# Kernel tuning notes

Hardware: AMD Instinct MI355X
Metric: run time of the kernel (lower is better)

## Reference

```python
import jax, jax.numpy as jnp
import numpy as np

N_NODES = 50000
N_EDGES = 400000
IN_DIM = 8
HIDDEN = 768
N_LAYERS = 4
LN_EPS = 1e-5


def setup_inputs() -> dict:
    key = jax.random.key(0)
    ks = jax.random.split(key, 10)
    x = jax.random.normal(ks[0], (N_NODES, IN_DIM), dtype=jnp.float32)
    edge_index = jax.random.randint(ks[1], (2, N_EDGES), 0, N_NODES, dtype=jnp.int32)
    # input projection
    s_in = 1.0 / np.sqrt(IN_DIM)
    Wp = jax.random.uniform(ks[2], (HIDDEN, IN_DIM), jnp.float32, -s_in, s_in)
    bp = jax.random.uniform(ks[3], (HIDDEN,), jnp.float32, -s_in, s_in)
    # stacked per-layer SAGEConv params (all layers have out_c == HIDDEN here)
    s_h = 1.0 / np.sqrt(HIDDEN)
    Wl = jax.random.uniform(ks[4], (N_LAYERS, HIDDEN, HIDDEN), jnp.float32, -s_h, s_h)  # lin_l (aggregated neighbors), has bias
    bl = jax.random.uniform(ks[5], (N_LAYERS, HIDDEN), jnp.float32, -s_h, s_h)
    Wr = jax.random.uniform(ks[6], (N_LAYERS, HIDDEN, HIDDEN), jnp.float32, -s_h, s_h)  # lin_r (root), no bias
    # LayerNorm params
    gamma = jnp.ones((N_LAYERS, HIDDEN), dtype=jnp.float32)
    beta = jnp.zeros((N_LAYERS, HIDDEN), dtype=jnp.float32)
    return {"x": x, "Wp": Wp, "bp": bp, "Wl": Wl, "bl": bl, "Wr": Wr,
            "gamma": gamma, "beta": beta, "edge_index": edge_index}


def _layer_norm(h, g, b):
    mu = jnp.mean(h, axis=-1, keepdims=True)
    var = jnp.mean(jnp.square(h - mu), axis=-1, keepdims=True)
    return (h - mu) * jax.lax.rsqrt(var + LN_EPS) * g + b


def reference(x, Wp, bp, Wl, bl, Wr, gamma, beta, edge_index):
    n = x.shape[0]
    src, dst = edge_index[0], edge_index[1]
    # in-degree per target node, clamped for mean
    deg = jax.ops.segment_sum(jnp.ones_like(dst, dtype=x.dtype), dst, num_segments=n)
    inv_deg = 1.0 / jnp.maximum(deg, 1.0)

    h = x @ Wp.T + bp  # [N, HIDDEN]

    def layer(h, params):
        Wl_i, bl_i, Wr_i, g_i, b_i = params
        # mean aggregation of source features at targets: [N, C]
        agg = jax.ops.segment_sum(h[src], dst, num_segments=n) * inv_deg[:, None]
        out = agg @ Wl_i.T + bl_i + h @ Wr_i.T  # SAGEConv
        out = _layer_norm(jax.nn.silu(out), g_i, b_i)  # norm(silu(conv))
        return out, None

    h, _ = jax.lax.scan(layer, h, (Wl, bl, Wr, gamma, beta))
    return h
```

## Files before the change

kernel.cpp:

```cpp
#include <hip/hip_runtime.h>

#define NN 50000
#define NE 400000
#define HID 768
#define NL 4

typedef short bf16x8_t __attribute__((ext_vector_type(8)));
typedef float f32x4_t __attribute__((ext_vector_type(4)));

__device__ __forceinline__ unsigned short f2bf(float f) {
  union { float f; unsigned int u; } c; c.f = f;
  unsigned int u = c.u;
  u += 0x7FFF + ((u >> 16) & 1);
  return (unsigned short)(u >> 16);
}
__device__ __forceinline__ float bf2f(unsigned short s) {
  union { unsigned int u; float f; } c; c.u = ((unsigned int)s) << 16;
  return c.f;
}

__global__ void k_zero2(int* __restrict__ a, int* __restrict__ b, int n) {
  int i = blockIdx.x * blockDim.x + threadIdx.x;
  if (i < n) { a[i] = 0; b[i] = 0; }
}

__global__ void k_cvt(const float* __restrict__ a, unsigned short* __restrict__ o, int n) {
  int i = blockIdx.x * blockDim.x + threadIdx.x;
  if (i < n) o[i] = f2bf(a[i]);
}

__global__ __launch_bounds__(256) void k_inproj(const float* __restrict__ x,
                                                const float* __restrict__ Wp,
                                                const float* __restrict__ bp,
                                                unsigned short* __restrict__ h) {
  int n = blockIdx.x;
  __shared__ float xs[8];
  if (threadIdx.x < 8) xs[threadIdx.x] = x[n * 8 + threadIdx.x];
  __syncthreads();
  for (int j = threadIdx.x; j < HID; j += 256) {
    const float* w = Wp + j * 8;
    float s = bp[j];
#pragma unroll
    for (int k = 0; k < 8; ++k) s += xs[k] * w[k];
    h[(size_t)n * HID + j] = f2bf(s);
  }
}

__global__ void k_deg(const int* __restrict__ dst, int* __restrict__ deg) {
  int i = blockIdx.x * blockDim.x + threadIdx.x;
  if (i < NE) atomicAdd(&deg[dst[i]], 1);
}

__global__ __launch_bounds__(1024) void k_scan(const int* __restrict__ deg, int* __restrict__ rowptr) {
  __shared__ int sm[1024];
  const int chunk = 49;
  int t = threadIdx.x;
  int start = t * chunk;
  int end = min(start + chunk, NN);
  int local = 0;
  for (int i = start; i < end; ++i) local += deg[i];
  sm[t] = local;
  __syncthreads();
  for (int off = 1; off < 1024; off <<= 1) {
    int v = (t >= off) ? sm[t - off] : 0;
    __syncthreads();
    sm[t] += v;
    __syncthreads();
  }
  int run = sm[t] - local;
  for (int i = start; i < end; ++i) { rowptr[i] = run; run += deg[i]; }
  if (start < NN && end == NN) rowptr[NN] = run;
}

__global__ void k_fill(const int* __restrict__ src, const int* __restrict__ dst,
                       const int* __restrict__ rowptr, int* __restrict__ cursor,
                       int* __restrict__ csr) {
  int i = blockIdx.x * blockDim.x + threadIdx.x;
  if (i < NE) {
    int d = dst[i];
    int pos = atomicAdd(&cursor[d], 1);
    csr[rowptr[d] + pos] = src[i];
  }
}

__global__ __launch_bounds__(192) void k_agg(const unsigned short* __restrict__ h,
                                             const int* __restrict__ csr,
                                             const int* __restrict__ rowptr,
                                             unsigned short* __restrict__ agg) {
  int n = blockIdx.x;
  int t = threadIdx.x;
  int beg = rowptr[n], end = rowptr[n + 1];
  float a0 = 0.f, a1 = 0.f, a2 = 0.f, a3 = 0.f;
  for (int i = beg; i < end; ++i) {
    int s = csr[i];
    ushort4 v = *(const ushort4*)(h + (size_t)s * HID + t * 4);
    a0 += bf2f(v.x); a1 += bf2f(v.y); a2 += bf2f(v.z); a3 += bf2f(v.w);
  }
  float inv = 1.0f / (float)max(end - beg, 1);
  ushort4 o;
  o.x = f2bf(a0 * inv); o.y = f2bf(a1 * inv); o.z = f2bf(a2 * inv); o.w = f2bf(a3 * inv);
  *(ushort4*)(agg + (size_t)n * HID + t * 4) = o;
}

#define BM 128
#define BN 128
#define BK 32
#define LST 40

__global__ __launch_bounds__(256) void k_gemm(const unsigned short* __restrict__ A0,
                                              const unsigned short* __restrict__ A1,
                                              const unsigned short* __restrict__ B0,
                                              const unsigned short* __restrict__ B1,
                                              const float* __restrict__ bias,
                                              float* __restrict__ out, int M) {
  __shared__ unsigned short As[BM * LST];
  __shared__ unsigned short Bs[BN * LST];
  f32x4_t acc[4][4] = {};
  int m0 = blockIdx.x * BM;
  int n0 = blockIdx.y * BN;
  int tid = threadIdx.x;
  int lane = tid & 63, w = tid >> 6;
  int wr = w >> 1, wc = w & 1;
  int srow = tid >> 2;
  int scol = (tid & 3) * 8;

  for (int phase = 0; phase < 2; ++phase) {
    const unsigned short* A = phase ? A1 : A0;
    const unsigned short* B = phase ? B1 : B0;
    for (int k0 = 0; k0 < HID; k0 += BK) {
      __syncthreads();
#pragma unroll
      for (int p = 0; p < 2; ++p) {
        int row = p * 64 + srow;
        int gm = m0 + row;
        int4 va;
        if (gm < M) va = *(const int4*)(A + (size_t)gm * HID + k0 + scol);
        else        va = int4{0, 0, 0, 0};
        *(int4*)(&As[row * LST + scol]) = va;
        int4 vb = *(const int4*)(B + (size_t)(n0 + row) * HID + k0 + scol);
        *(int4*)(&Bs[row * LST + scol]) = vb;
      }
      __syncthreads();
      bf16x8_t af[4], bf[4];
      int kq = (lane >> 4) * 8;
      int mr = lane & 15;
#pragma unroll
      for (int t = 0; t < 4; ++t) {
        af[t] = *(const bf16x8_t*)(&As[(wr * 64 + t * 16 + mr) * LST + kq]);
        bf[t] = *(const bf16x8_t*)(&Bs[(wc * 64 + t * 16 + mr) * LST + kq]);
      }
#pragma unroll
      for (int mt = 0; mt < 4; ++mt)
#pragma unroll
        for (int nt = 0; nt < 4; ++nt)
          acc[mt][nt] = __builtin_amdgcn_mfma_f32_16x16x32_bf16(af[mt], bf[nt], acc[mt][nt], 0, 0, 0);
    }
  }
  int col = lane & 15;
  int rq = (lane >> 4) * 4;
#pragma unroll
  for (int mt = 0; mt < 4; ++mt) {
#pragma unroll
    for (int nt = 0; nt < 4; ++nt) {
      int j = n0 + wc * 64 + nt * 16 + col;
      float b = bias[j];
#pragma unroll
      for (int r = 0; r < 4; ++r) {
        int gm = m0 + wr * 64 + mt * 16 + rq + r;
        if (gm < M) out[(size_t)gm * HID + j] = acc[mt][nt][r] + b;
      }
    }
  }
}

__global__ __launch_bounds__(256) void k_siluln(const float* __restrict__ pre,
                                                const float* __restrict__ gamma,
                                                const float* __restrict__ beta,
                                                unsigned short* __restrict__ hout,
                                                float* __restrict__ fout) {
  int n = blockIdx.x;
  const float* p = pre + (size_t)n * HID;
  float v[3];
  float sum = 0.f, sq = 0.f;
#pragma unroll
  for (int i = 0; i < 3; ++i) {
    float x = p[threadIdx.x + i * 256];
    float s = x / (1.f + __expf(-x));
    v[i] = s; sum += s; sq += s * s;
  }
#pragma unroll
  for (int off = 32; off >= 1; off >>= 1) {
    sum += __shfl_down(sum, off);
    sq  += __shfl_down(sq, off);
  }
  __shared__ float rs[4], rq2[4];
  int wv = threadIdx.x >> 6;
  if ((threadIdx.x & 63) == 0) { rs[wv] = sum; rq2[wv] = sq; }
  __syncthreads();
  if (threadIdx.x == 0) {
    float s = rs[0] + rs[1] + rs[2] + rs[3];
    float q = rq2[0] + rq2[1] + rq2[2] + rq2[3];
    rs[0] = s / (float)HID;
    rq2[0] = q / (float)HID;
  }
  __syncthreads();
  float mu = rs[0];
  float var = rq2[0] - mu * mu;
  float inv = rsqrtf(var + 1e-5f);
#pragma unroll
  for (int i = 0; i < 3; ++i) {
    int j = threadIdx.x + i * 256;
    float y = (v[i] - mu) * inv * gamma[j] + beta[j];
    if (fout) fout[(size_t)n * HID + j] = y;
    else      hout[(size_t)n * HID + j] = f2bf(y);
  }
}

extern "C" void kernel_launch(void* const* d_in, const int* in_sizes, int n_in,
                              void* d_out, int out_size, void* d_ws, size_t ws_size,
                              hipStream_t stream) {
  const float* x     = (const float*)d_in[0];
  const float* Wp    = (const float*)d_in[1];
  const float* bp    = (const float*)d_in[2];
  const float* Wl    = (const float*)d_in[3];
  const float* bl    = (const float*)d_in[4];
  const float* Wr    = (const float*)d_in[5];
  const float* gamma = (const float*)d_in[6];
  const float* beta  = (const float*)d_in[7];
  const int*   ei    = (const int*)d_in[8];
  float* out = (float*)d_out;

  const int* src = ei;
  const int* dst = ei + NE;

  char* p = (char*)d_ws;
  unsigned short* h    = (unsigned short*)p;              p += (size_t)NN * HID * 2;
  unsigned short* agg  = (unsigned short*)p;              p += (size_t)NN * HID * 2;
  float* pre           = (float*)p;                       p += (size_t)NN * HID * 4;
  unsigned short* Wlb  = (unsigned short*)p;              p += (size_t)NL * HID * HID * 2;
  unsigned short* Wrb  = (unsigned short*)p;              p += (size_t)NL * HID * HID * 2;
  int* deg             = (int*)p;                         p += (size_t)NN * 4;
  int* rowptr          = (int*)p;                         p += (size_t)(NN + 1) * 4 + 12;
  int* cursor          = (int*)p;                         p += (size_t)NN * 4;
  int* csr             = (int*)p;                         p += (size_t)NE * 4;

  k_zero2<<<(NN + 255) / 256, 256, 0, stream>>>(deg, cursor, NN);
  int wn = NL * HID * HID;
  k_cvt<<<(wn + 255) / 256, 256, 0, stream>>>(Wl, Wlb, wn);
  k_cvt<<<(wn + 255) / 256, 256, 0, stream>>>(Wr, Wrb, wn);
  k_inproj<<<NN, 256, 0, stream>>>(x, Wp, bp, h);
  k_deg<<<(NE + 255) / 256, 256, 0, stream>>>(dst, deg);
  k_scan<<<1, 1024, 0, stream>>>(deg, rowptr);
  k_fill<<<(NE + 255) / 256, 256, 0, stream>>>(src, dst, rowptr, cursor, csr);

  dim3 ggrid((NN + BM - 1) / BM, HID / BN);
  for (int l = 0; l < NL; ++l) {
    k_agg<<<NN, 192, 0, stream>>>(h, csr, rowptr, agg);
    k_gemm<<<ggrid, 256, 0, stream>>>(agg, h,
                                      Wlb + (size_t)l * HID * HID,
                                      Wrb + (size_t)l * HID * HID,
                                      bl + (size_t)l * HID, pre, NN);
    k_siluln<<<NN, 256, 0, stream>>>(pre, gamma + (size_t)l * HID, beta + (size_t)l * HID,
                                     h, (l == NL - 1) ? out : nullptr);
  }
}
```

Before: 1.983 ms.

## Fuse SiLU into GEMM epilogue, store bf16 activations, async LDS tile loads

```diff
diff --git a/kernel.cpp b/kernel.cpp
--- a/kernel.cpp
+++ b/kernel.cpp
@@ -17,6 +17,12 @@
 __device__ __forceinline__ float bf2f(unsigned short s) {
   union { unsigned int u; float f; } c; c.u = ((unsigned int)s) << 16;
   return c.f;
+}
+
+__device__ __forceinline__ void async16(const void* g, void* l) {
+  __builtin_amdgcn_global_load_lds((const __attribute__((address_space(1))) void*)g,
+                                   (__attribute__((address_space(3))) void*)l,
+                                   16, 0, 0);
 }
 
 __global__ void k_zero2(int* __restrict__ a, int* __restrict__ b, int n) {
@@ -105,24 +111,23 @@
 #define BM 128
 #define BN 128
 #define BK 32
-#define LST 40
 
 __global__ __launch_bounds__(256) void k_gemm(const unsigned short* __restrict__ A0,
                                               const unsigned short* __restrict__ A1,
                                               const unsigned short* __restrict__ B0,
                                               const unsigned short* __restrict__ B1,
                                               const float* __restrict__ bias,
-                                              float* __restrict__ out, int M) {
-  __shared__ unsigned short As[BM * LST];
-  __shared__ unsigned short Bs[BN * LST];
+                                              unsigned short* __restrict__ sact, int M) {
+  __shared__ unsigned short As[BM * BK];
+  __shared__ unsigned short Bs[BN * BK];
   f32x4_t acc[4][4] = {};
-  int m0 = blockIdx.x * BM;
-  int n0 = blockIdx.y * BN;
+  int n0 = blockIdx.x * BN;
+  int m0 = blockIdx.y * BM;
   int tid = threadIdx.x;
   int lane = tid & 63, w = tid >> 6;
   int wr = w >> 1, wc = w & 1;
-  int srow = tid >> 2;
-  int scol = (tid & 3) * 8;
+  int r4 = lane >> 2;
+  int cs = (lane & 3) * 8;
 
   for (int phase = 0; phase < 2; ++phase) {
     const unsigned short* A = phase ? A1 : A0;
@@ -130,30 +135,26 @@
     for (int k0 = 0; k0 < HID; k0 += BK) {
       __syncthreads();
 #pragma unroll
-      for (int p = 0; p < 2; ++p) {
-        int row = p * 64 + srow;
-        int gm = m0 + row;
-        int4 va;
-        if (gm < M) va = *(const int4*)(A + (size_t)gm * HID + k0 + scol);
-        else        va = int4{0, 0, 0, 0};
-        *(int4*)(&As[row * LST + scol]) = va;
-        int4 vb = *(const int4*)(B + (size_t)(n0 + row) * HID + k0 + scol);
-        *(int4*)(&Bs[row * LST + scol]) = vb;
+      for (int c = 0; c < 2; ++c) {
+        int seg = w * 32 + c * 16;
+        int row = seg + r4;
+        async16(A + (size_t)(m0 + row) * HID + k0 + cs, &As[seg * BK]);
+        async16(B + (size_t)(n0 + row) * HID + k0 + cs, &Bs[seg * BK]);
       }
       __syncthreads();
-      bf16x8_t af[4], bf[4];
+      bf16x8_t af[4], bfr[4];
       int kq = (lane >> 4) * 8;
       int mr = lane & 15;
 #pragma unroll
       for (int t = 0; t < 4; ++t) {
-        af[t] = *(const bf16x8_t*)(&As[(wr * 64 + t * 16 + mr) * LST + kq]);
-        bf[t] = *(const bf16x8_t*)(&Bs[(wc * 64 + t * 16 + mr) * LST + kq]);
+        af[t]  = *(const bf16x8_t*)(&As[(wr * 64 + t * 16 + mr) * BK + kq]);
+        bfr[t] = *(const bf16x8_t*)(&Bs[(wc * 64 + t * 16 + mr) * BK + kq]);
       }
 #pragma unroll
       for (int mt = 0; mt < 4; ++mt)
 #pragma unroll
         for (int nt = 0; nt < 4; ++nt)
-          acc[mt][nt] = __builtin_amdgcn_mfma_f32_16x16x32_bf16(af[mt], bf[nt], acc[mt][nt], 0, 0, 0);
+          acc[mt][nt] = __builtin_amdgcn_mfma_f32_16x16x32_bf16(af[mt], bfr[nt], acc[mt][nt], 0, 0, 0);
     }
   }
   int col = lane & 15;
@@ -167,25 +168,28 @@
 #pragma unroll
       for (int r = 0; r < 4; ++r) {
         int gm = m0 + wr * 64 + mt * 16 + rq + r;
-        if (gm < M) out[(size_t)gm * HID + j] = acc[mt][nt][r] + b;
+        if (gm < M) {
+          float v = acc[mt][nt][r] + b;
+          float s = v / (1.f + __expf(-v));
+          sact[(size_t)gm * HID + j] = f2bf(s);
+        }
       }
     }
   }
 }
 
-__global__ __launch_bounds__(256) void k_siluln(const float* __restrict__ pre,
-                                                const float* __restrict__ gamma,
-                                                const float* __restrict__ beta,
-                                                unsigned short* __restrict__ hout,
-                                                float* __restrict__ fout) {
+__global__ __launch_bounds__(256) void k_ln(const unsigned short* __restrict__ sact,
+                                            const float* __restrict__ gamma,
+                                            const float* __restrict__ beta,
+                                            unsigned short* __restrict__ hout,
+                                            float* __restrict__ fout) {
   int n = blockIdx.x;
-  const float* p = pre + (size_t)n * HID;
+  const unsigned short* p = sact + (size_t)n * HID;
   float v[3];
   float sum = 0.f, sq = 0.f;
 #pragma unroll
   for (int i = 0; i < 3; ++i) {
-    float x = p[threadIdx.x + i * 256];
-    float s = x / (1.f + __expf(-x));
+    float s = bf2f(p[threadIdx.x + i * 256]);
     v[i] = s; sum += s; sq += s * s;
   }
 #pragma unroll
@@ -236,7 +240,7 @@
   char* p = (char*)d_ws;
   unsigned short* h    = (unsigned short*)p;              p += (size_t)NN * HID * 2;
   unsigned short* agg  = (unsigned short*)p;              p += (size_t)NN * HID * 2;
-  float* pre           = (float*)p;                       p += (size_t)NN * HID * 4;
+  unsigned short* sact = (unsigned short*)p;              p += (size_t)NN * HID * 2;
   unsigned short* Wlb  = (unsigned short*)p;              p += (size_t)NL * HID * HID * 2;
   unsigned short* Wrb  = (unsigned short*)p;              p += (size_t)NL * HID * HID * 2;
   int* deg             = (int*)p;                         p += (size_t)NN * 4;
@@ -253,14 +257,14 @@
   k_scan<<<1, 1024, 0, stream>>>(deg, rowptr);
   k_fill<<<(NE + 255) / 256, 256, 0, stream>>>(src, dst, rowptr, cursor, csr);
 
-  dim3 ggrid((NN + BM - 1) / BM, HID / BN);
+  dim3 ggrid(HID / BN, (NN + BM - 1) / BM);
   for (int l = 0; l < NL; ++l) {
     k_agg<<<NN, 192, 0, stream>>>(h, csr, rowptr, agg);
     k_gemm<<<ggrid, 256, 0, stream>>>(agg, h,
                                       Wlb + (size_t)l * HID * HID,
                                       Wrb + (size_t)l * HID * HID,
-                                      bl + (size_t)l * HID, pre, NN);
-    k_siluln<<<NN, 256, 0, stream>>>(pre, gamma + (size_t)l * HID, beta + (size_t)l * HID,
-                                     h, (l == NL - 1) ? out : nullptr);
-  }
-}
+                                      bl + (size_t)l * HID, sact, NN);
+    k_ln<<<NN, 256, 0, stream>>>(sact, gamma + (size_t)l * HID, beta + (size_t)l * HID,
+                                 h, (l == NL - 1) ? out : nullptr);
+  }
+}
```

Measured after the change: 1.794 ms. -9.5%, faster.
